# Kernel tuning notes

Measured on AMD Instinct MI355X. Metric: run time of the kernel, lower is better.

The kernel has to match this reference:

```python
import jax, jax.numpy as jnp
import numpy as np

N_STREAMS = 4
SINKHORN_ITERS = 20
EPS = 1e-8


def sinkhorn_knopp(log_mat, num_iters=SINKHORN_ITERS, eps=EPS):
    mat = jnp.exp(log_mat)
    def body(_, m):
        m = m / (m.sum(axis=-2, keepdims=True) + eps)
        m = m / (m.sum(axis=-1, keepdims=True) + eps)
        return m
    return jax.lax.fori_loop(0, num_iters, body, mat)


def setup_inputs() -> dict:
    key = jax.random.key(0)
    B, L, C = 4, 2048, 1024
    n = N_STREAMS
    hidden = 4 * C
    ks = jax.random.split(key, 8)
    def xavier(k, shape):
        fan_in, fan_out = shape[0], shape[1]
        lim = np.sqrt(6.0 / (fan_in + fan_out))
        return jax.random.uniform(k, shape, jnp.float32, -lim, lim)
    return {
        "x": jax.random.normal(ks[0], (B, L, C), jnp.float32),
        "rms_weight": jnp.ones((C * n,), jnp.float32),
        "W_dyn": xavier(ks[1], (C * n, n * n + 2 * n)),  # Linear no-bias, stored [in,out]
        "bias_pre": jnp.zeros((1, n), jnp.float32),
        "bias_post": jnp.zeros((1, n), jnp.float32),
        "bias_res": jnp.zeros((n, n), jnp.float32),
        "alpha_pre": jnp.full((1,), 0.01, jnp.float32),
        "alpha_post": jnp.full((1,), 0.01, jnp.float32),
        "alpha_res": jnp.full((1,), 0.01, jnp.float32),
        "W1": xavier(ks[2], (C, hidden)),
        "b1": jnp.zeros((hidden,), jnp.float32),
        "W2": xavier(ks[3], (hidden, C)),
        "b2": jnp.zeros((C,), jnp.float32),
        "Wout": xavier(ks[4], (C * n, C)),
        "bout": jnp.zeros((C,), jnp.float32),
    }


def reference(x, rms_weight, W_dyn, bias_pre, bias_post, bias_res,
              alpha_pre, alpha_post, alpha_res, W1, b1, W2, b2, Wout, bout):
    B, L, C = x.shape
    n = bias_pre.shape[1]
    # x expanded across streams (broadcast view, no copy)
    x_exp = jnp.broadcast_to(x[:, :, None, :], (B, L, n, C))  # [B,L,n,C]
    x_flat = x_exp.reshape(B, L, n * C)
    # RMSNorm
    rms = jnp.sqrt(jnp.mean(x_flat * x_flat, axis=-1, keepdims=True) + EPS)
    x_norm = x_flat / rms * rms_weight
    # dynamic projection
    dynamic = x_norm @ W_dyn  # [B,L,n*n+2n]
    dyn_pre = dynamic[..., :n]
    dyn_post = dynamic[..., n:2 * n]
    dyn_res = dynamic[..., 2 * n:].reshape(B, L, n, n)
    H_pre = jax.nn.sigmoid(alpha_pre * dyn_pre + bias_pre)            # [B,L,n]
    H_post = 2.0 * jax.nn.sigmoid(alpha_post * dyn_post + bias_post)  # [B,L,n]
    H_res = sinkhorn_knopp(alpha_res * dyn_res + bias_res)            # [B,L,n,n]
    # pre-mix streams then residual MLP
    pre_mixed = jnp.einsum('bln,blnc->blc', H_pre, x_exp)
    h = jax.nn.gelu(pre_mixed @ W1 + b1, approximate=False)
    f_out = h @ W2 + b2  # [B,L,C]
    # post mixing + doubly-stochastic residual mixing
    post_mixed = H_post[..., None] * f_out[:, :, None, :]             # [B,L,n,C]
    res_mixed = jnp.einsum('blnm,blmc->blnc', H_res, x_exp)
    merged = (res_mixed + post_mixed).reshape(B, L, n * C)
    return merged @ Wout + bout + x
```

## Files before the change

### kernel.cpp

```cpp
#include <hip/hip_runtime.h>

typedef unsigned short u16;
typedef __bf16 bf16x8 __attribute__((ext_vector_type(8)));
typedef float f32x4 __attribute__((ext_vector_type(4)));

__device__ __forceinline__ u16 f2bf(float f) {
  unsigned int u = __builtin_bit_cast(unsigned int, f);
  u += 0x7fffu + ((u >> 16) & 1u);
  return (u16)(u >> 16);
}

__device__ __forceinline__ void gload_lds16(const u16* g, u16* l) {
  __builtin_amdgcn_global_load_lds((const __attribute__((address_space(1))) unsigned int*)g,
                                   (__attribute__((address_space(3))) unsigned int*)l,
                                   16, 0, 0);
}

__device__ __forceinline__ float gelu_erf(float v) {
  const float z = v * 0.70710678118654752f;
  const float az = fabsf(z);
  const float t = __builtin_amdgcn_rcpf(1.0f + 0.3275911f * az);
  const float p = t * (0.254829592f +
                  t * (-0.284496736f +
                  t * (1.421413741f +
                  t * (-1.453152027f + t * 1.061405429f))));
  const float e = __expf(-az * az);
  float er = 1.0f - p * e;
  er = (z < 0.f) ? -er : er;
  return 0.5f * v * (1.0f + er);
}


__global__ __launch_bounds__(256) void weff_kernel(const float* __restrict__ rmsw,
                                                   const float* __restrict__ Wdyn,
                                                   float* __restrict__ WT) {
  int idx = blockIdx.x * 256 + threadIdx.x;
  int j = idx >> 10, c = idx & 1023;
  float s = 0.f;
#pragma unroll
  for (int st = 0; st < 4; ++st) {
    int r = st * 1024 + c;
    s += rmsw[r] * Wdyn[(long)r * 24 + j];
  }
  WT[idx] = s;
}

__global__ __launch_bounds__(256) void pack_all(const float* __restrict__ W1,
                                                const float* __restrict__ W2,
                                                const float* __restrict__ WO,
                                                u16* __restrict__ F1,
                                                u16* __restrict__ F2,
                                                u16* __restrict__ FO) {
  const int blk = blockIdx.x;
  const int sel = blk >> 11;
  const float* W;
  u16* FMB;
  int lgN, KC;
  if (sel == 0)      { W = W1; FMB = F1; lgN = 12; KC = 32; }
  else if (sel == 1) { W = W2; FMB = F2; lgN = 10; KC = 128; }
  else               { W = WO; FMB = FO; lgN = 10; KC = 128; }
  const long gid = (long)(blk & 2047) * 256 + threadIdx.x;
  const int N = 1 << lgN;
  const int n = (int)(gid & (N - 1));
  const int k0 = (int)(gid >> lgN) * 8;
  unsigned int p[4];
#pragma unroll
  for (int d = 0; d < 4; ++d) {
    const float lo = W[(long)(k0 + 2 * d) * N + n];
    const float hi = W[(long)(k0 + 2 * d + 1) * N + n];
    p[d] = (unsigned)f2bf(lo) | ((unsigned)f2bf(hi) << 16);
  }
  const long ad = ((long)(n >> 4) * KC + (k0 >> 5)) * 512 +
                  ((n & 15) + (((k0 >> 3) & 3) << 4)) * 8;
  *(uint4*)(FMB + ad) = make_uint4(p[0], p[1], p[2], p[3]);
}

__global__ __launch_bounds__(512) void prep_tokens(
    const float* __restrict__ x, const float* __restrict__ WT,
    const float* __restrict__ bias_pre, const float* __restrict__ bias_post,
    const float* __restrict__ bias_res, const float* __restrict__ a_pre,
    const float* __restrict__ a_post, const float* __restrict__ a_res,
    u16* __restrict__ preA, float* __restrict__ scal) {
  const int tid = threadIdx.x;
  const int b = blockIdx.x;
  const long t0 = (long)b * 16;

  __shared__ float red[32][16][26];
  __shared__ float tot2[16][26];
  __shared__ float spre[16];

  {
    const int tt = tid & 15;
    const int cc = tid >> 4;
    const float* xp = x + (t0 + tt) * 1024 + cc * 32;
    float part[25];
#pragma unroll
    for (int j = 0; j < 25; ++j) part[j] = 0.f;
#pragma unroll
    for (int g = 0; g < 8; ++g) {
      const float4 xv = *(const float4*)(xp + g * 4);
      part[24] += xv.x * xv.x + xv.y * xv.y + xv.z * xv.z + xv.w * xv.w;
#pragma unroll
      for (int j = 0; j < 24; ++j) {
        const float4 wv = *(const float4*)(WT + (long)j * 1024 + cc * 32 + g * 4);
        part[j] += xv.x * wv.x + xv.y * wv.y + xv.z * wv.z + xv.w * wv.w;
      }
    }
#pragma unroll
    for (int j = 0; j < 25; ++j) red[cc][tt][j] = part[j];
  }
  __syncthreads();

  {
    const int tt = tid >> 5;
    const int j = tid & 31;
    if (j < 25) {
      float s = 0.f;
#pragma unroll
      for (int cc = 0; cc < 32; ++cc) s += red[cc][tt][j];
      tot2[tt][j] = s;
    }
  }
  __syncthreads();

  if (tid < 256) {
    const int tt = tid >> 4;
    const int m = tid & 15;
    const long t = t0 + tt;
    const float rms = sqrtf(tot2[tt][24] * (1.0f / 1024.0f) + 1e-8f);
    const float rinv = 1.0f / rms;

    if (m == 0) {
      const float ap = a_pre[0];
      float s_pre = 0.f;
#pragma unroll
      for (int i = 0; i < 4; ++i)
        s_pre += 1.f / (1.f + expf(-(ap * tot2[tt][i] * rinv + bias_pre[i])));
      spre[tt] = s_pre;
    }
    if (m < 4) {
      const float apo = a_post[0];
      float hp = 2.f / (1.f + expf(-(apo * tot2[tt][4 + m] * rinv + bias_post[m])));
      scal[t * 8 + 4 + m] = hp;
    }
    const float ar = a_res[0];
    float Mv = expf(ar * tot2[tt][8 + m] * rinv + bias_res[m]);
#pragma unroll
    for (int it = 0; it < 20; ++it) {
      float cs = Mv + __shfl_xor(Mv, 4);
      cs += __shfl_xor(cs, 8);
      Mv = Mv / (cs + 1e-8f);
      float rs = Mv + __shfl_xor(Mv, 1);
      rs += __shfl_xor(rs, 2);
      Mv = Mv / (rs + 1e-8f);
    }
    float rs = Mv + __shfl_xor(Mv, 1);
    rs += __shfl_xor(rs, 2);
    if ((m & 3) == 0) scal[t * 8 + (m >> 2)] = rs;
  }
  __syncthreads();

  {
    const int w = tid >> 6;
    const int lane = tid & 63;
    const int tl = lane & 15;
    const int co = (lane >> 4) * 8;
    const float sp = spre[tl];
#pragma unroll
    for (int p = 0; p < 4; ++p) {
      const int ki = p * 8 + w;
      const float* xr = x + (t0 + tl) * 1024 + ki * 32 + co;
      const float4 xa = *(const float4*)(xr);
      const float4 xb = *(const float4*)(xr + 4);
      unsigned q0 = (unsigned)f2bf(sp * xa.x) | ((unsigned)f2bf(sp * xa.y) << 16);
      unsigned q1 = (unsigned)f2bf(sp * xa.z) | ((unsigned)f2bf(sp * xa.w) << 16);
      unsigned q2 = (unsigned)f2bf(sp * xb.x) | ((unsigned)f2bf(sp * xb.y) << 16);
      unsigned q3 = (unsigned)f2bf(sp * xb.z) | ((unsigned)f2bf(sp * xb.w) << 16);
      *(uint4*)(preA + ((long)b * 32 + ki) * 512 + lane * 8) = make_uint4(q0, q1, q2, q3);
    }
  }
}

__global__ __launch_bounds__(256, 2) void gemm_fm1(const u16* __restrict__ A,
                                                   const u16* __restrict__ B,
                                                   const float* __restrict__ bias,
                                                   u16* __restrict__ dst) {
  const int tid = threadIdx.x;
  const int lane = tid & 63;
  const int wave = tid >> 6;
  const int wm = wave >> 1, wn = wave & 1;
  const int b = blockIdx.x;
  const int c = b & 7, u = b >> 3;
  const int p = u >> 5, v = u & 31;
  const int by = (p * 2 + (c >> 2)) * 4 + (v >> 3);
  const int bx = (c & 3) * 8 + (v & 7);

  __shared__ u16 lds[4][16][512];
  u16* const l0 = (u16*)lds;

  const u16* gb[4];
#pragma unroll
  for (int l = 0; l < 4; ++l) {
    const int t = wave * 4 + l;
    gb[l] = (t < 8) ? (A + ((long)(by * 8 + t) * 32) * 512 + lane * 8)
                    : (B + ((long)(bx * 8 + (t - 8)) * 32) * 512 + lane * 8);
  }

#define STG(kt)                                                              \
  {                                                                          \
    u16* cb_ = l0 + (((kt) & 3) * 16 + wave * 4) * 512;                      \
    const long ko_ = (long)(kt)*512;                                         \
    _Pragma("unroll") for (int l_ = 0; l_ < 4; ++l_)                         \
        gload_lds16(gb[l_] + ko_, cb_ + l_ * 512);                           \
  }

  f32x4 acc[4][4] = {};

  STG(0); STG(1); STG(2);
  asm volatile("s_waitcnt vmcnt(8)" ::: "memory");
  __builtin_amdgcn_s_barrier();

  for (int kt = 0; kt < 32; ++kt) {
    if (kt + 3 < 32) STG(kt + 3);
    const u16* cb = l0 + (kt & 3) * (16 * 512);
    bf16x8 af[4], bf[4];
#pragma unroll
    for (int i = 0; i < 4; ++i)
      af[i] = *(const bf16x8*)(cb + (wm * 4 + i) * 512 + lane * 8);
#pragma unroll
    for (int j = 0; j < 4; ++j)
      bf[j] = *(const bf16x8*)(cb + (8 + wn * 4 + j) * 512 + lane * 8);
    asm volatile("s_waitcnt lgkmcnt(0)" ::: "memory");
    __builtin_amdgcn_sched_barrier(0);
    __builtin_amdgcn_s_setprio(1);
#pragma unroll
    for (int i = 0; i < 4; ++i)
#pragma unroll
      for (int j = 0; j < 4; ++j)
        acc[i][j] = __builtin_amdgcn_mfma_f32_16x16x32_bf16(af[i], bf[j], acc[i][j], 0, 0, 0);
    __builtin_amdgcn_s_setprio(0);
    if (kt + 4 <= 32)      asm volatile("s_waitcnt vmcnt(8)" ::: "memory");
    else if (kt + 3 == 32) asm volatile("s_waitcnt vmcnt(4)" ::: "memory");
    else                   asm volatile("s_waitcnt vmcnt(0)" ::: "memory");
    __builtin_amdgcn_s_barrier();
  }
#undef STG

  u16* ep = l0 + wave * 4096;
#pragma unroll
  for (int i = 0; i < 4; ++i)
#pragma unroll
    for (int j = 0; j < 4; ++j) {
      const int col = bx * 128 + wn * 64 + j * 16 + (lane & 15);
      const float bcol = bias[col];
#pragma unroll
      for (int r = 0; r < 4; ++r) {
        const float g = gelu_erf(acc[i][j][r] + bcol);
        const int lp = ((lane >> 4) * 4 + r) | ((((j & 1) << 1) | ((lane & 15) >> 3)) << 4);
        ep[(i * 2 + (j >> 1)) * 512 + lp * 8 + (lane & 7)] = f2bf(g);
      }
    }
#pragma unroll
  for (int ch = 0; ch < 8; ++ch) {
    const int i = ch >> 1, jc = ch & 1;
    const long row16 = by * 8 + wm * 4 + i;
    const long col32 = bx * 4 + wn * 2 + jc;
    *(uint4*)(dst + (row16 * 128 + col32) * 512 + lane * 8) =
        *(const uint4*)(ep + ch * 512 + lane * 8);
  }
}

template <int EPI, int NT, int SWZ, int LGGX>
__global__ __launch_bounds__(512, 2) void gemm_fm2(const u16* __restrict__ A,
                                                   const u16* __restrict__ B,
                                                   const int KCtot, const int KCout,
                                                   const float* __restrict__ bias,
                                                   const float* __restrict__ X,
                                                   const float* __restrict__ scal,
                                                   void* __restrict__ dstv) {
  constexpr int CH = 16 + NT;
  constexpr int SC = CH / 8;
  constexpr int AI = (NT == 16) ? 8 : 4;
  const int tid = threadIdx.x;
  const int lane = tid & 63;
  const int wave = tid >> 6;
  const int wm = (NT == 16) ? (wave >> 2) : (wave >> 1);
  const int wn = (NT == 16) ? (wave & 3) : (wave & 1);
  const int b = blockIdx.x;
  int bx, by;
  if constexpr (SWZ == 1) {
    const int c = b & 7, u = b >> 3;
    const int p = u >> 5, v = u & 31;
    by = (p * 2 + (c >> 2)) * 4 + (v >> 3);
    bx = (c & 3) * 8 + (v & 7);
  } else {
    const int c = b & 7, s = b >> 3;
    bx = s & ((1 << LGGX) - 1);
    by = c * 4 + (s >> LGGX);
  }

  __shared__ u16 lds[4][CH][512];
  u16* const l0 = (u16*)lds;

  const u16* gb[4];
#pragma unroll
  for (int l = 0; l < SC; ++l) {
    const int t = wave * SC + l;
    gb[l] = (t < 16) ? (A + ((long)(by * 16 + t) * KCtot) * 512 + lane * 8)
                     : (B + ((long)(bx * NT + (t - 16)) * KCtot) * 512 + lane * 8);
  }

#define STG(kt)                                                              \
  {                                                                          \
    u16* cb_ = l0 + (((kt) & 3) * CH + wave * SC) * 512;                     \
    const long ko_ = (long)(kt)*512;                                         \
    _Pragma("unroll") for (int l_ = 0; l_ < SC; ++l_)                        \
        gload_lds16(gb[l_] + ko_, cb_ + l_ * 512);                           \
  }

  f32x4 acc[AI][4] = {};

  STG(0); STG(1); STG(2);
  if constexpr (SC == 4) asm volatile("s_waitcnt vmcnt(8)" ::: "memory");
  else                   asm volatile("s_waitcnt vmcnt(6)" ::: "memory");
  __builtin_amdgcn_s_barrier();

  for (int kt = 0; kt < KCtot; ++kt) {
    if (kt + 3 < KCtot) STG(kt + 3);
    const u16* cb = l0 + (kt & 3) * (CH * 512);
    bf16x8 af[AI], bf[4];
#pragma unroll
    for (int i = 0; i < AI; ++i)
      af[i] = *(const bf16x8*)(cb + (wm * AI + i) * 512 + lane * 8);
#pragma unroll
    for (int j = 0; j < 4; ++j)
      bf[j] = *(const bf16x8*)(cb + (16 + wn * 4 + j) * 512 + lane * 8);
    asm volatile("s_waitcnt lgkmcnt(0)" ::: "memory");
    __builtin_amdgcn_sched_barrier(0);
    __builtin_amdgcn_s_setprio(1);
#pragma unroll
    for (int i = 0; i < AI; ++i)
#pragma unroll
      for (int j = 0; j < 4; ++j)
        acc[i][j] = __builtin_amdgcn_mfma_f32_16x16x32_bf16(af[i], bf[j], acc[i][j], 0, 0, 0);
    __builtin_amdgcn_s_setprio(0);
    if (kt + 4 <= KCtot) {
      if constexpr (SC == 4) asm volatile("s_waitcnt vmcnt(8)" ::: "memory");
      else                   asm volatile("s_waitcnt vmcnt(6)" ::: "memory");
    } else if (kt + 3 == KCtot) {
      if constexpr (SC == 4) asm volatile("s_waitcnt vmcnt(4)" ::: "memory");
      else                   asm volatile("s_waitcnt vmcnt(3)" ::: "memory");
    } else {
      asm volatile("s_waitcnt vmcnt(0)" ::: "memory");
    }
    __builtin_amdgcn_s_barrier();
  }
#undef STG

  if constexpr (EPI == 1) {
    u16* dst = (u16*)dstv;
    u16* ep = l0 + wave * 4096;
#pragma unroll
    for (int i = 0; i < AI; ++i) {
      float rr[4][4], hh[4][4];
#pragma unroll
      for (int r = 0; r < 4; ++r) {
        const int row = by * 256 + wm * 64 + i * 16 + (lane >> 4) * 4 + r;
        const float4 rv = *(const float4*)(scal + (long)row * 8);
        const float4 hv = *(const float4*)(scal + (long)row * 8 + 4);
        rr[r][0] = rv.x; rr[r][1] = rv.y; rr[r][2] = rv.z; rr[r][3] = rv.w;
        hh[r][0] = hv.x; hh[r][1] = hv.y; hh[r][2] = hv.z; hh[r][3] = hv.w;
      }
#pragma unroll
      for (int jc = 0; jc < 2; ++jc) {
#pragma unroll
        for (int jj = 0; jj < 2; ++jj) {
          const int j = jc * 2 + jj;
          const int col = bx * 128 + wn * 64 + j * 16 + (lane & 15);
          const float bcol = bias[col];
#pragma unroll
          for (int r = 0; r < 4; ++r) {
            const int row = by * 256 + wm * 64 + i * 16 + (lane >> 4) * 4 + r;
            const float f = acc[i][j][r] + bcol;
            const float xval = X[(long)row * 1024 + col];
            const int lp = ((lane >> 4) * 4 + r) | (((jj << 1) | ((lane & 15) >> 3)) << 4);
#pragma unroll
            for (int ss = 0; ss < 4; ++ss)
              ep[ss * 512 + lp * 8 + (lane & 7)] = f2bf(rr[r][ss] * xval + hh[r][ss] * f);
          }
        }
        const long row16 = by * 16 + wm * 4 + i;
        const long col32 = bx * 4 + wn * 2 + jc;
#pragma unroll
        for (int ss = 0; ss < 4; ++ss)
          *(uint4*)(dst + (row16 * 128 + (long)ss * 32 + col32) * 512 + lane * 8) =
              *(const uint4*)(ep + ss * 512 + lane * 8);
      }
    }
  } else {
    float* dst = (float*)dstv;
    float* ep32 = (float*)(l0 + wave * 4096);
#pragma unroll
    for (int half = 0; half < 2; ++half) {
#pragma unroll
      for (int i2 = 0; i2 < 2; ++i2) {
        const int i = half * 2 + i2;
#pragma unroll
        for (int j = 0; j < 4; ++j) {
          const int col = bx * 128 + wn * 64 + j * 16 + (lane & 15);
          const float bcol = bias[col];
#pragma unroll
          for (int r = 0; r < 4; ++r) {
            const long row = by * 256 + wm * 64 + i * 16 + (lane >> 4) * 4 + r;
            ep32[(i2 * 16 + (lane >> 4) * 4 + r) * 64 + j * 16 + (lane & 15)] =
                acc[i][j][r] + bcol + X[row * 1024 + col];
          }
        }
      }
#pragma unroll
      for (int q = 0; q < 8; ++q) {
        const int lr = q * 4 + (lane >> 4);
        const long row = by * 256 + wm * 64 + half * 32 + lr;
        const long col = bx * 128 + wn * 64 + (lane & 15) * 4;
        *(float4*)(dst + row * 1024 + col) =
            *(const float4*)(ep32 + lr * 64 + (lane & 15) * 4);
      }
    }
  }
}

extern "C" void kernel_launch(void* const* d_in, const int* in_sizes, int n_in,
                              void* d_out, int out_size, void* d_ws, size_t ws_size,
                              hipStream_t stream) {
  (void)in_sizes; (void)n_in; (void)out_size; (void)ws_size;
  const float* x = (const float*)d_in[0];
  const float* rmsw = (const float*)d_in[1];
  const float* Wdyn = (const float*)d_in[2];
  const float* bias_pre = (const float*)d_in[3];
  const float* bias_post = (const float*)d_in[4];
  const float* bias_res = (const float*)d_in[5];
  const float* a_pre = (const float*)d_in[6];
  const float* a_post = (const float*)d_in[7];
  const float* a_res = (const float*)d_in[8];
  const float* W1 = (const float*)d_in[9];
  const float* b1 = (const float*)d_in[10];
  const float* W2 = (const float*)d_in[11];
  const float* b2 = (const float*)d_in[12];
  const float* Wout = (const float*)d_in[13];
  const float* bout = (const float*)d_in[14];
  float* out = (float*)d_out;
  char* ws = (char*)d_ws;

  constexpr size_t MB = 1048576;
  u16* W1fm = (u16*)(ws);
  u16* W2fm = (u16*)(ws + 8 * MB);
  u16* WOfm = (u16*)(ws + 16 * MB);
  float* WT = (float*)(ws + 24 * MB);
  float* scal = (float*)(ws + 24 * MB + 98304);
  u16* h = (u16*)(ws + 25 * MB);
  u16* merged = (u16*)(ws + 89 * MB);
  u16* preA = (u16*)(ws + 89 * MB);

  weff_kernel<<<96, 256, 0, stream>>>(rmsw, Wdyn, WT);
  pack_all<<<6144, 256, 0, stream>>>(W1, W2, Wout, W1fm, W2fm, WOfm);
  prep_tokens<<<512, 512, 0, stream>>>(x, WT, bias_pre, bias_post, bias_res,
                                       a_pre, a_post, a_res, preA, scal);
  gemm_fm1<<<2048, 256, 0, stream>>>(preA, W1fm, b1, h);
  gemm_fm2<1, 8, 0, 3><<<256, 512, 0, stream>>>(h, W2fm, 128, 128, b2, x, scal, merged);
  gemm_fm2<2, 8, 0, 3><<<256, 512, 0, stream>>>(merged, WOfm, 128, 0, bout, x, nullptr, out);
}
```

Before: 426.0 us.

## Merge weight-effective kernel into packing launch and restructure token prep with LDS staging

Folds the small weff computation into the weight-packing kernel as extra blocks, removing one launch. The token-prep kernel now handles 32 tokens per 256-thread block and stages x panels in padded shared memory, so each WT load is reused across 32 tokens instead of 16. This cuts redundant global WT reads but adds LDS traffic and barriers, and halves the grid to 256 blocks, which may lower occupancy.

```diff
diff --git a/kernel.cpp b/kernel.cpp
--- a/kernel.cpp
+++ b/kernel.cpp
@@ -31,27 +31,28 @@
 }
 
 
-__global__ __launch_bounds__(256) void weff_kernel(const float* __restrict__ rmsw,
-                                                   const float* __restrict__ Wdyn,
-                                                   float* __restrict__ WT) {
-  int idx = blockIdx.x * 256 + threadIdx.x;
-  int j = idx >> 10, c = idx & 1023;
-  float s = 0.f;
-#pragma unroll
-  for (int st = 0; st < 4; ++st) {
-    int r = st * 1024 + c;
-    s += rmsw[r] * Wdyn[(long)r * 24 + j];
-  }
-  WT[idx] = s;
-}
-
-__global__ __launch_bounds__(256) void pack_all(const float* __restrict__ W1,
-                                                const float* __restrict__ W2,
-                                                const float* __restrict__ WO,
-                                                u16* __restrict__ F1,
-                                                u16* __restrict__ F2,
-                                                u16* __restrict__ FO) {
+__global__ __launch_bounds__(256) void pack_weff(const float* __restrict__ W1,
+                                                 const float* __restrict__ W2,
+                                                 const float* __restrict__ WO,
+                                                 u16* __restrict__ F1,
+                                                 u16* __restrict__ F2,
+                                                 u16* __restrict__ FO,
+                                                 const float* __restrict__ rmsw,
+                                                 const float* __restrict__ Wdyn,
+                                                 float* __restrict__ WT) {
   const int blk = blockIdx.x;
+  if (blk >= 6144) {
+    int idx = (blk - 6144) * 256 + threadIdx.x;
+    int j = idx >> 10, c = idx & 1023;
+    float s = 0.f;
+#pragma unroll
+    for (int st = 0; st < 4; ++st) {
+      int r = st * 1024 + c;
+      s += rmsw[r] * Wdyn[(long)r * 24 + j];
+    }
+    WT[idx] = s;
+    return;
+  }
   const int sel = blk >> 11;
   const float* W;
   u16* FMB;
@@ -75,7 +76,7 @@
   *(uint4*)(FMB + ad) = make_uint4(p[0], p[1], p[2], p[3]);
 }
 
-__global__ __launch_bounds__(512) void prep_tokens(
+__global__ __launch_bounds__(256) void prep_tokens(
     const float* __restrict__ x, const float* __restrict__ WT,
     const float* __restrict__ bias_pre, const float* __restrict__ bias_post,
     const float* __restrict__ bias_res, const float* __restrict__ a_pre,
@@ -83,51 +84,76 @@
     u16* __restrict__ preA, float* __restrict__ scal) {
   const int tid = threadIdx.x;
   const int b = blockIdx.x;
-  const long t0 = (long)b * 16;
-
-  __shared__ float red[32][16][26];
-  __shared__ float tot2[16][26];
-  __shared__ float spre[16];
+  const long t0 = (long)b * 32;
+
+  __shared__ float xs[32 * 257];
+  __shared__ float red[8][32][26];
+  __shared__ float tot2[32][26];
+  __shared__ float spre[32];
+
+  const int tt = tid & 31;
+  const int q = tid >> 5;
+
+  float part[25];
+#pragma unroll
+  for (int j = 0; j < 25; ++j) part[j] = 0.f;
+
+  for (int panel = 0; panel < 4; ++panel) {
+    const int cb = panel * 256;
+#pragma unroll
+    for (int pass = 0; pass < 8; ++pass) {
+      const int idx = pass * 256 + tid;
+      const int row = idx >> 6;
+      const int c4 = (idx & 63) * 4;
+      const float4 v = *(const float4*)(x + (t0 + row) * 1024 + cb + c4);
+      xs[row * 257 + c4 + 0] = v.x;
+      xs[row * 257 + c4 + 1] = v.y;
+      xs[row * 257 + c4 + 2] = v.z;
+      xs[row * 257 + c4 + 3] = v.w;
+    }
+    __syncthreads();
+#pragma unroll 2
+    for (int g = 0; g < 8; ++g) {
+      const int cl = q * 32 + g * 4;
+      float xv0 = xs[tt * 257 + cl + 0];
+      float xv1 = xs[tt * 257 + cl + 1];
+      float xv2 = xs[tt * 257 + cl + 2];
+      float xv3 = xs[tt * 257 + cl + 3];
+      const float* wp = WT + cb + cl;
+#pragma unroll
+      for (int j = 0; j < 24; ++j) {
+        const float4 wv = *(const float4*)(wp + j * 1024);
+        part[j] += xv0 * wv.x + xv1 * wv.y + xv2 * wv.z + xv3 * wv.w;
+      }
+      part[24] += xv0 * xv0 + xv1 * xv1 + xv2 * xv2 + xv3 * xv3;
+    }
+    __syncthreads();
+  }
+
+#pragma unroll
+  for (int j = 0; j < 25; ++j) red[q][tt][j] = part[j];
+  __syncthreads();
 
   {
-    const int tt = tid & 15;
-    const int cc = tid >> 4;
-    const float* xp = x + (t0 + tt) * 1024 + cc * 32;
-    float part[25];
-#pragma unroll
-    for (int j = 0; j < 25; ++j) part[j] = 0.f;
-#pragma unroll
-    for (int g = 0; g < 8; ++g) {
-      const float4 xv = *(const float4*)(xp + g * 4);
-      part[24] += xv.x * xv.x + xv.y * xv.y + xv.z * xv.z + xv.w * xv.w;
-#pragma unroll
-      for (int j = 0; j < 24; ++j) {
-        const float4 wv = *(const float4*)(WT + (long)j * 1024 + cc * 32 + g * 4);
-        part[j] += xv.x * wv.x + xv.y * wv.y + xv.z * wv.z + xv.w * wv.w;
-      }
-    }
-#pragma unroll
-    for (int j = 0; j < 25; ++j) red[cc][tt][j] = part[j];
+    const int jj = tid >> 5;
+#pragma unroll
+    for (int k = 0; k < 4; ++k) {
+      const int j = jj + 8 * k;
+      if (j < 25) {
+        float s = 0.f;
+#pragma unroll
+        for (int qq = 0; qq < 8; ++qq) s += red[qq][tt][j];
+        tot2[tt][j] = s;
+      }
+    }
   }
   __syncthreads();
 
-  {
-    const int tt = tid >> 5;
-    const int j = tid & 31;
-    if (j < 25) {
-      float s = 0.f;
-#pragma unroll
-      for (int cc = 0; cc < 32; ++cc) s += red[cc][tt][j];
-      tot2[tt][j] = s;
-    }
-  }
-  __syncthreads();
-
-  if (tid < 256) {
-    const int tt = tid >> 4;
+  for (int it = 0; it < 2; ++it) {
+    const int tg = it * 16 + (tid >> 4);
     const int m = tid & 15;
-    const long t = t0 + tt;
-    const float rms = sqrtf(tot2[tt][24] * (1.0f / 1024.0f) + 1e-8f);
+    const long t = t0 + tg;
+    const float rms = sqrtf(tot2[tg][24] * (1.0f / 1024.0f) + 1e-8f);
     const float rinv = 1.0f / rms;
 
     if (m == 0) {
@@ -135,18 +161,18 @@
       float s_pre = 0.f;
 #pragma unroll
       for (int i = 0; i < 4; ++i)
-        s_pre += 1.f / (1.f + expf(-(ap * tot2[tt][i] * rinv + bias_pre[i])));
-      spre[tt] = s_pre;
+        s_pre += 1.f / (1.f + expf(-(ap * tot2[tg][i] * rinv + bias_pre[i])));
+      spre[tg] = s_pre;
     }
     if (m < 4) {
       const float apo = a_post[0];
-      float hp = 2.f / (1.f + expf(-(apo * tot2[tt][4 + m] * rinv + bias_post[m])));
+      float hp = 2.f / (1.f + expf(-(apo * tot2[tg][4 + m] * rinv + bias_post[m])));
       scal[t * 8 + 4 + m] = hp;
     }
     const float ar = a_res[0];
-    float Mv = expf(ar * tot2[tt][8 + m] * rinv + bias_res[m]);
-#pragma unroll
-    for (int it = 0; it < 20; ++it) {
+    float Mv = expf(ar * tot2[tg][8 + m] * rinv + bias_res[m]);
+#pragma unroll
+    for (int si = 0; si < 20; ++si) {
       float cs = Mv + __shfl_xor(Mv, 4);
       cs += __shfl_xor(cs, 8);
       Mv = Mv / (cs + 1e-8f);
@@ -163,20 +189,23 @@
   {
     const int w = tid >> 6;
     const int lane = tid & 63;
+    const int rg = w & 1;
+    const int kh = (w >> 1) * 16;
     const int tl = lane & 15;
     const int co = (lane >> 4) * 8;
-    const float sp = spre[tl];
-#pragma unroll
-    for (int p = 0; p < 4; ++p) {
-      const int ki = p * 8 + w;
-      const float* xr = x + (t0 + tl) * 1024 + ki * 32 + co;
+    const float sp = spre[rg * 16 + tl];
+#pragma unroll
+    for (int kk = 0; kk < 16; ++kk) {
+      const int ki = kh + kk;
+      const float* xr = x + (t0 + rg * 16 + tl) * 1024 + ki * 32 + co;
       const float4 xa = *(const float4*)(xr);
       const float4 xb = *(const float4*)(xr + 4);
       unsigned q0 = (unsigned)f2bf(sp * xa.x) | ((unsigned)f2bf(sp * xa.y) << 16);
       unsigned q1 = (unsigned)f2bf(sp * xa.z) | ((unsigned)f2bf(sp * xa.w) << 16);
       unsigned q2 = (unsigned)f2bf(sp * xb.x) | ((unsigned)f2bf(sp * xb.y) << 16);
       unsigned q3 = (unsigned)f2bf(sp * xb.z) | ((unsigned)f2bf(sp * xb.w) << 16);
-      *(uint4*)(preA + ((long)b * 32 + ki) * 512 + lane * 8) = make_uint4(q0, q1, q2, q3);
+      *(uint4*)(preA + ((long)(b * 2 + rg) * 32 + ki) * 512 + lane * 8) =
+          make_uint4(q0, q1, q2, q3);
     }
   }
 }
@@ -461,9 +490,8 @@
   u16* merged = (u16*)(ws + 89 * MB);
   u16* preA = (u16*)(ws + 89 * MB);
 
-  weff_kernel<<<96, 256, 0, stream>>>(rmsw, Wdyn, WT);
-  pack_all<<<6144, 256, 0, stream>>>(W1, W2, Wout, W1fm, W2fm, WOfm);
-  prep_tokens<<<512, 512, 0, stream>>>(x, WT, bias_pre, bias_post, bias_res,
+  pack_weff<<<6240, 256, 0, stream>>>(W1, W2, Wout, W1fm, W2fm, WOfm, rmsw, Wdyn, WT);
+  prep_tokens<<<256, 256, 0, stream>>>(x, WT, bias_pre, bias_post, bias_res,
                                        a_pre, a_post, a_res, preA, scal);
   gemm_fm1<<<2048, 256, 0, stream>>>(preA, W1fm, b1, h);
   gemm_fm2<1, 8, 0, 3><<<256, 512, 0, stream>>>(h, W2fm, 128, 128, b2, x, scal, merged);
```

After: 418.1 us. No clear change (-1.9%).
